# Optimization experiments

Measured on AMD Instinct MI355X. Metric: run time of the kernel, lower is better.

Reference implementation:

```python
import jax, jax.numpy as jnp
import numpy as np

DELTA_INF = 1e10  # delta appended for the last sample, as in the torch code
EPS = 1e-10


def setup_inputs() -> dict:
    key = jax.random.key(0)
    k1, k2, k3 = jax.random.split(key, 3)
    N, S = 131072, 192
    ray_samples = jax.random.normal(k1, (N, S, 3), dtype=jnp.float32)
    densities = jax.random.normal(k2, (N, S, 1), dtype=jnp.float32)
    rgb = jax.random.uniform(k3, (N, S, 3), dtype=jnp.float32)
    background_color = jnp.ones((3,), dtype=jnp.float32)
    return {"ray_samples": ray_samples, "densities": densities, "rgb": rgb,
            "background_color": background_color}


def _render_weights(ray_samples, densities):
    # delta_i = ||x_{i+1} - x_i||, last delta = 1e10  -> [N, S, 1]
    diff = ray_samples[..., 1:, :] - ray_samples[..., :-1, :]
    delta = jnp.linalg.norm(diff, axis=-1, keepdims=True)
    delta = jnp.concatenate(
        [delta, jnp.full_like(delta[..., -1:, :], DELTA_INF)], axis=-2)
    alpha = 1.0 - jnp.exp(-jax.nn.relu(densities) * delta)
    # transmittance T_i = prod_{j<i} (1 - alpha_j + eps), exclusive cumprod
    trans = jnp.cumprod(
        jnp.concatenate(
            [jnp.ones_like(alpha[..., :1, :]), 1.0 - alpha + EPS], axis=-2),
        axis=-2)[..., :-1, :]
    weights = alpha * trans  # [N, S, 1]
    return weights


def reference(ray_samples, densities, rgb, background_color):
    weights = _render_weights(ray_samples, densities)
    rendered_rgb = jnp.sum(weights * rgb, axis=-2)           # [N, 3]
    accumulated_alpha = jnp.sum(weights, axis=-2)            # [N, 1]
    # composite with background: img + bg * (1 - acc)
    rendered_rgb = rendered_rgb + background_color * (1.0 - accumulated_alpha)
    return rendered_rgb, accumulated_alpha[..., 0], weights
```

## Files before the change

kernel.cpp:

```cpp
#include <hip/hip_runtime.h>

constexpr int NRAYS = 131072;
constexpr float DELTA_INF_F = 1e10f;
constexpr float EPS_F = 1e-10f;
constexpr int GRID  = 2048;
constexpr int BLOCK = 256;
constexpr int WAVES = GRID * (BLOCK / 64);
constexpr int ITERS = NRAYS / WAVES;

__global__ __launch_bounds__(256) void nerf_render_kernel(
    const float4* __restrict__ rsF4,
    const float4* __restrict__ denF4,
    const float4* __restrict__ rgbF4,
    const float* __restrict__ bg,
    float* __restrict__ out_rgb,
    float* __restrict__ out_acc,
    float4* __restrict__ out_wF4)
{
    const int lane = threadIdx.x & 63;
    const int gw   = (int)((blockIdx.x * BLOCK + threadIdx.x) >> 6);
    const bool act = lane < 48;
    const float bg0 = bg[0], bg1 = bg[1], bg2 = bg[2];
    const float4 Z = make_float4(0.f, 0.f, 0.f, 0.f);

    int ray = gw;
    float4 P0 = Z, P1 = Z, P2 = Z, D = Z, C0 = Z, C1 = Z, C2 = Z;
    if (act) {
        const float4* rp = rsF4 + (size_t)ray * 144 + 3 * lane;
        P0 = rp[0]; P1 = rp[1]; P2 = rp[2];
        D = denF4[(size_t)ray * 48 + lane];
        const float4* rc = rgbF4 + (size_t)ray * 144 + 3 * lane;
        C0 = rc[0]; C1 = rc[1]; C2 = rc[2];
    }

#pragma unroll 2
    for (int it = 0; it < ITERS; ++it) {
        int nray = ray + WAVES;
        float4 nP0 = Z, nP1 = Z, nP2 = Z, nD = Z, nC0 = Z, nC1 = Z, nC2 = Z;
        if (act && (it + 1 < ITERS)) {
            const float4* rp = rsF4 + (size_t)nray * 144 + 3 * lane;
            nP0 = rp[0]; nP1 = rp[1]; nP2 = rp[2];
            nD = denF4[(size_t)nray * 48 + lane];
            const float4* rc = rgbF4 + (size_t)nray * 144 + 3 * lane;
            nC0 = rc[0]; nC1 = rc[1]; nC2 = rc[2];
        }

        float x0 = P0.x, y0 = P0.y, z0 = P0.z;
        float x1 = P0.w, y1 = P1.x, z1 = P1.y;
        float x2 = P1.z, y2 = P1.w, z2 = P2.x;
        float x3 = P2.y, y3 = P2.z, z3 = P2.w;

        float nx = __shfl_down(x0, 1);
        float ny = __shfl_down(y0, 1);
        float nz = __shfl_down(z0, 1);

        float dx = x1 - x0, dy = y1 - y0, dz = z1 - z0;
        float d0 = sqrtf(dx * dx + dy * dy + dz * dz);
        dx = x2 - x1; dy = y2 - y1; dz = z2 - z1;
        float d1 = sqrtf(dx * dx + dy * dy + dz * dz);
        dx = x3 - x2; dy = y3 - y2; dz = z3 - z2;
        float d2 = sqrtf(dx * dx + dy * dy + dz * dz);
        dx = nx - x3; dy = ny - y3; dz = nz - z3;
        float d3 = (lane == 47) ? DELTA_INF_F : sqrtf(dx * dx + dy * dy + dz * dz);

        float e0 = __expf(-fmaxf(D.x, 0.f) * d0);
        float e1 = __expf(-fmaxf(D.y, 0.f) * d1);
        float e2 = __expf(-fmaxf(D.z, 0.f) * d2);
        float e3 = __expf(-fmaxf(D.w, 0.f) * d3);
        float a0 = 1.f - e0, a1 = 1.f - e1, a2 = 1.f - e2, a3 = 1.f - e3;
        float t0 = (1.f - a0) + EPS_F;
        float t1 = (1.f - a1) + EPS_F;
        float t2 = (1.f - a2) + EPS_F;
        float t3 = (1.f - a3) + EPS_F;

        float t01 = t0 * t1;
        float t012 = t01 * t2;
        float incl = t012 * t3;
#pragma unroll
        for (int off = 1; off < 64; off <<= 1) {
            float t = __shfl_up(incl, off);
            if (lane >= off) incl *= t;
        }
        float pref = __shfl_up(incl, 1);
        if (lane == 0) pref = 1.f;

        float w0 = a0 * pref;
        float w1 = a1 * pref * t0;
        float w2 = a2 * pref * t01;
        float w3 = a3 * pref * t012;
        float acc = w0 + w1 + w2 + w3;

        if (act)
            out_wF4[(size_t)ray * 48 + lane] = make_float4(w0, w1, w2, w3);

        float cr = w0 * C0.x + w1 * C0.w + w2 * C1.z + w3 * C2.y;
        float cg = w0 * C0.y + w1 * C1.x + w2 * C1.w + w3 * C2.z;
        float cb = w0 * C0.z + w1 * C1.y + w2 * C2.x + w3 * C2.w;

#pragma unroll
        for (int off = 32; off >= 1; off >>= 1) {
            cr  += __shfl_xor(cr, off);
            cg  += __shfl_xor(cg, off);
            cb  += __shfl_xor(cb, off);
            acc += __shfl_xor(acc, off);
        }

        if (lane == 0) {
            float om = 1.f - acc;
            out_rgb[(size_t)ray * 3 + 0] = cr + bg0 * om;
            out_rgb[(size_t)ray * 3 + 1] = cg + bg1 * om;
            out_rgb[(size_t)ray * 3 + 2] = cb + bg2 * om;
            out_acc[ray] = acc;
        }

        P0 = nP0; P1 = nP1; P2 = nP2; D = nD; C0 = nC0; C1 = nC1; C2 = nC2;
        ray = nray;
    }
}

extern "C" void kernel_launch(void* const* d_in, const int* in_sizes, int n_in,
                              void* d_out, int out_size, void* d_ws, size_t ws_size,
                              hipStream_t stream) {
    const float4* rsF4  = (const float4*)d_in[0];
    const float4* denF4 = (const float4*)d_in[1];
    const float4* rgbF4 = (const float4*)d_in[2];
    const float*  bg    = (const float*)d_in[3];

    float* o = (float*)d_out;
    float*  out_rgb = o;
    float*  out_acc = o + (size_t)NRAYS * 3;
    float4* out_wF4 = (float4*)(o + (size_t)NRAYS * 4);

    dim3 grid(GRID), block(BLOCK);
    hipLaunchKernelGGL(nerf_render_kernel, grid, block, 0, stream,
                       rsF4, denF4, rgbF4, bg, out_rgb, out_acc, out_wF4);
}
```

Measured before the change: 170.2 us.

## Launch one wave per ray and use nontemporal stores for outputs

Drops the persistent grid-stride loop with software prefetch and launches one 64-lane wave per ray, giving 32768 blocks of 256 threads. Outputs are now written with nontemporal stores to avoid polluting the cache with streaming data. This trades explicit prefetch pipelining for more waves in flight to hide memory latency, at the cost of extra block launch overhead and repeated loads of the background colour.

```diff
diff --git a/kernel.cpp b/kernel.cpp
--- a/kernel.cpp
+++ b/kernel.cpp
@@ -3,10 +3,8 @@
 constexpr int NRAYS = 131072;
 constexpr float DELTA_INF_F = 1e10f;
 constexpr float EPS_F = 1e-10f;
-constexpr int GRID  = 2048;
-constexpr int BLOCK = 256;
-constexpr int WAVES = GRID * (BLOCK / 64);
-constexpr int ITERS = NRAYS / WAVES;
+
+typedef float floatx4 __attribute__((ext_vector_type(4)));
 
 __global__ __launch_bounds__(256) void nerf_render_kernel(
     const float4* __restrict__ rsF4,
@@ -18,12 +16,10 @@
     float4* __restrict__ out_wF4)
 {
     const int lane = threadIdx.x & 63;
-    const int gw   = (int)((blockIdx.x * BLOCK + threadIdx.x) >> 6);
+    const int ray  = (blockIdx.x << 2) + (threadIdx.x >> 6);
     const bool act = lane < 48;
-    const float bg0 = bg[0], bg1 = bg[1], bg2 = bg[2];
     const float4 Z = make_float4(0.f, 0.f, 0.f, 0.f);
 
-    int ray = gw;
     float4 P0 = Z, P1 = Z, P2 = Z, D = Z, C0 = Z, C1 = Z, C2 = Z;
     if (act) {
         const float4* rp = rsF4 + (size_t)ray * 144 + 3 * lane;
@@ -33,88 +29,75 @@
         C0 = rc[0]; C1 = rc[1]; C2 = rc[2];
     }
 
-#pragma unroll 2
-    for (int it = 0; it < ITERS; ++it) {
-        int nray = ray + WAVES;
-        float4 nP0 = Z, nP1 = Z, nP2 = Z, nD = Z, nC0 = Z, nC1 = Z, nC2 = Z;
-        if (act && (it + 1 < ITERS)) {
-            const float4* rp = rsF4 + (size_t)nray * 144 + 3 * lane;
-            nP0 = rp[0]; nP1 = rp[1]; nP2 = rp[2];
-            nD = denF4[(size_t)nray * 48 + lane];
-            const float4* rc = rgbF4 + (size_t)nray * 144 + 3 * lane;
-            nC0 = rc[0]; nC1 = rc[1]; nC2 = rc[2];
-        }
+    float x0 = P0.x, y0 = P0.y, z0 = P0.z;
+    float x1 = P0.w, y1 = P1.x, z1 = P1.y;
+    float x2 = P1.z, y2 = P1.w, z2 = P2.x;
+    float x3 = P2.y, y3 = P2.z, z3 = P2.w;
 
-        float x0 = P0.x, y0 = P0.y, z0 = P0.z;
-        float x1 = P0.w, y1 = P1.x, z1 = P1.y;
-        float x2 = P1.z, y2 = P1.w, z2 = P2.x;
-        float x3 = P2.y, y3 = P2.z, z3 = P2.w;
+    float nx = __shfl_down(x0, 1);
+    float ny = __shfl_down(y0, 1);
+    float nz = __shfl_down(z0, 1);
 
-        float nx = __shfl_down(x0, 1);
-        float ny = __shfl_down(y0, 1);
-        float nz = __shfl_down(z0, 1);
+    float dx = x1 - x0, dy = y1 - y0, dz = z1 - z0;
+    float d0 = sqrtf(dx * dx + dy * dy + dz * dz);
+    dx = x2 - x1; dy = y2 - y1; dz = z2 - z1;
+    float d1 = sqrtf(dx * dx + dy * dy + dz * dz);
+    dx = x3 - x2; dy = y3 - y2; dz = z3 - z2;
+    float d2 = sqrtf(dx * dx + dy * dy + dz * dz);
+    dx = nx - x3; dy = ny - y3; dz = nz - z3;
+    float d3 = (lane == 47) ? DELTA_INF_F : sqrtf(dx * dx + dy * dy + dz * dz);
 
-        float dx = x1 - x0, dy = y1 - y0, dz = z1 - z0;
-        float d0 = sqrtf(dx * dx + dy * dy + dz * dz);
-        dx = x2 - x1; dy = y2 - y1; dz = z2 - z1;
-        float d1 = sqrtf(dx * dx + dy * dy + dz * dz);
-        dx = x3 - x2; dy = y3 - y2; dz = z3 - z2;
-        float d2 = sqrtf(dx * dx + dy * dy + dz * dz);
-        dx = nx - x3; dy = ny - y3; dz = nz - z3;
-        float d3 = (lane == 47) ? DELTA_INF_F : sqrtf(dx * dx + dy * dy + dz * dz);
+    float e0 = __expf(-fmaxf(D.x, 0.f) * d0);
+    float e1 = __expf(-fmaxf(D.y, 0.f) * d1);
+    float e2 = __expf(-fmaxf(D.z, 0.f) * d2);
+    float e3 = __expf(-fmaxf(D.w, 0.f) * d3);
+    float a0 = 1.f - e0, a1 = 1.f - e1, a2 = 1.f - e2, a3 = 1.f - e3;
+    float t0 = (1.f - a0) + EPS_F;
+    float t1 = (1.f - a1) + EPS_F;
+    float t2 = (1.f - a2) + EPS_F;
+    float t3 = (1.f - a3) + EPS_F;
 
-        float e0 = __expf(-fmaxf(D.x, 0.f) * d0);
-        float e1 = __expf(-fmaxf(D.y, 0.f) * d1);
-        float e2 = __expf(-fmaxf(D.z, 0.f) * d2);
-        float e3 = __expf(-fmaxf(D.w, 0.f) * d3);
-        float a0 = 1.f - e0, a1 = 1.f - e1, a2 = 1.f - e2, a3 = 1.f - e3;
-        float t0 = (1.f - a0) + EPS_F;
-        float t1 = (1.f - a1) + EPS_F;
-        float t2 = (1.f - a2) + EPS_F;
-        float t3 = (1.f - a3) + EPS_F;
+    float t01 = t0 * t1;
+    float t012 = t01 * t2;
+    float incl = t012 * t3;
+#pragma unroll
+    for (int off = 1; off < 64; off <<= 1) {
+        float t = __shfl_up(incl, off);
+        if (lane >= off) incl *= t;
+    }
+    float pref = __shfl_up(incl, 1);
+    if (lane == 0) pref = 1.f;
 
-        float t01 = t0 * t1;
-        float t012 = t01 * t2;
-        float incl = t012 * t3;
-#pragma unroll
-        for (int off = 1; off < 64; off <<= 1) {
-            float t = __shfl_up(incl, off);
-            if (lane >= off) incl *= t;
-        }
-        float pref = __shfl_up(incl, 1);
-        if (lane == 0) pref = 1.f;
+    float w0 = a0 * pref;
+    float w1 = a1 * pref * t0;
+    float w2 = a2 * pref * t01;
+    float w3 = a3 * pref * t012;
+    float acc = w0 + w1 + w2 + w3;
 
-        float w0 = a0 * pref;
-        float w1 = a1 * pref * t0;
-        float w2 = a2 * pref * t01;
-        float w3 = a3 * pref * t012;
-        float acc = w0 + w1 + w2 + w3;
+    if (act) {
+        floatx4 wv = {w0, w1, w2, w3};
+        __builtin_nontemporal_store(wv,
+            (floatx4*)(out_wF4 + (size_t)ray * 48 + lane));
+    }
 
-        if (act)
-            out_wF4[(size_t)ray * 48 + lane] = make_float4(w0, w1, w2, w3);
-
-        float cr = w0 * C0.x + w1 * C0.w + w2 * C1.z + w3 * C2.y;
-        float cg = w0 * C0.y + w1 * C1.x + w2 * C1.w + w3 * C2.z;
-        float cb = w0 * C0.z + w1 * C1.y + w2 * C2.x + w3 * C2.w;
+    float cr = w0 * C0.x + w1 * C0.w + w2 * C1.z + w3 * C2.y;
+    float cg = w0 * C0.y + w1 * C1.x + w2 * C1.w + w3 * C2.z;
+    float cb = w0 * C0.z + w1 * C1.y + w2 * C2.x + w3 * C2.w;
 
 #pragma unroll
-        for (int off = 32; off >= 1; off >>= 1) {
-            cr  += __shfl_xor(cr, off);
-            cg  += __shfl_xor(cg, off);
-            cb  += __shfl_xor(cb, off);
-            acc += __shfl_xor(acc, off);
-        }
+    for (int off = 32; off >= 1; off >>= 1) {
+        cr  += __shfl_xor(cr, off);
+        cg  += __shfl_xor(cg, off);
+        cb  += __shfl_xor(cb, off);
+        acc += __shfl_xor(acc, off);
+    }
 
-        if (lane == 0) {
-            float om = 1.f - acc;
-            out_rgb[(size_t)ray * 3 + 0] = cr + bg0 * om;
-            out_rgb[(size_t)ray * 3 + 1] = cg + bg1 * om;
-            out_rgb[(size_t)ray * 3 + 2] = cb + bg2 * om;
-            out_acc[ray] = acc;
-        }
-
-        P0 = nP0; P1 = nP1; P2 = nP2; D = nD; C0 = nC0; C1 = nC1; C2 = nC2;
-        ray = nray;
+    if (lane == 0) {
+        float om = 1.f - acc;
+        __builtin_nontemporal_store(cr + bg[0] * om, out_rgb + (size_t)ray * 3 + 0);
+        __builtin_nontemporal_store(cg + bg[1] * om, out_rgb + (size_t)ray * 3 + 1);
+        __builtin_nontemporal_store(cb + bg[2] * om, out_rgb + (size_t)ray * 3 + 2);
+        __builtin_nontemporal_store(acc, out_acc + ray);
     }
 }
 
@@ -131,7 +114,7 @@
     float*  out_acc = o + (size_t)NRAYS * 3;
     float4* out_wF4 = (float4*)(o + (size_t)NRAYS * 4);
 
-    dim3 grid(GRID), block(BLOCK);
+    dim3 grid(NRAYS / 4), block(256);
     hipLaunchKernelGGL(nerf_render_kernel, grid, block, 0, stream,
                        rsF4, denF4, rgbF4, bg, out_rgb, out_acc, out_wF4);
 }
```

After: 147.5 us. -13.3%, faster.
